# Kernel optimization log

Measured on AMD Instinct MI355X. Metric: run time of the kernel, lower is better.

Reference implementation:

```python
import jax, jax.numpy as jnp
import numpy as np
import math

MAX_P = 150
D_MODEL = 128
N_HEADS = 4
D_HEAD = D_MODEL // N_HEADS
D_MLP = 512
D_MEM = 64
VOCAB = MAX_P + 2  # 152
EQ_TOKEN = MAX_P + 1  # 151
B = 65536


def setup_inputs() -> dict:
    key = jax.random.key(0)
    ks = jax.random.split(key, 20)
    s = 1.0 / math.sqrt(D_MODEL)
    inp = {
        "p_val": jax.random.randint(ks[0], (B,), 0, MAX_P),
        "a": jax.random.randint(ks[1], (B,), 0, MAX_P),
        "b": jax.random.randint(ks[2], (B,), 0, MAX_P),
        # embeddings
        "token_embed": jax.random.normal(ks[3], (VOCAB, D_MODEL), jnp.float32),
        "pos_embed": jax.random.normal(ks[4], (5, D_MODEL), jnp.float32),
        # TitansMemory
        "W_mem": jax.random.normal(ks[5], (D_MODEL, D_MEM), jnp.float32) * s,
        "b_mem": jnp.zeros((D_MEM,), jnp.float32),
        "W_sur": jax.random.normal(ks[6], (D_MEM, D_MODEL), jnp.float32) * (1.0 / math.sqrt(D_MEM)),
        "b_sur": jnp.zeros((D_MODEL,), jnp.float32),
        "W_m2r": jax.random.normal(ks[7], (D_MEM, D_MODEL), jnp.float32) * (1.0 / math.sqrt(D_MEM)),
        "b_m2r": jnp.zeros((D_MODEL,), jnp.float32),
        # attention
        "W_Q": jax.random.normal(ks[8], (N_HEADS, D_MODEL, D_HEAD), jnp.float32) * s,
        "W_K": jax.random.normal(ks[9], (N_HEADS, D_MODEL, D_HEAD), jnp.float32) * s,
        "W_V": jax.random.normal(ks[10], (N_HEADS, D_MODEL, D_HEAD), jnp.float32) * s,
        "W_O": jax.random.normal(ks[11], (N_HEADS, D_HEAD, D_MODEL), jnp.float32) * s,
        # MLP
        "W_mlp1": jax.random.normal(ks[12], (D_MODEL, D_MLP), jnp.float32) * s,
        "b_mlp1": jnp.zeros((D_MLP,), jnp.float32),
        "W_mlp2": jax.random.normal(ks[13], (D_MLP, D_MODEL), jnp.float32) * (1.0 / math.sqrt(D_MLP)),
        "b_mlp2": jnp.zeros((D_MODEL,), jnp.float32),
        # unembed
        "W_un": jax.random.normal(ks[14], (D_MODEL, MAX_P), jnp.float32) * s,
        "b_un": jnp.zeros((MAX_P,), jnp.float32),
    }
    return inp


def reference(p_val, a, b, token_embed, pos_embed, W_mem, b_mem, W_sur, b_sur,
              W_m2r, b_m2r, W_Q, W_K, W_V, W_O, W_mlp1, b_mlp1, W_mlp2, b_mlp2,
              W_un, b_un):
    eq = jnp.full_like(a, EQ_TOKEN)
    tokens = jnp.stack([p_val, a, b, eq], axis=1)            # [B, 4]
    x = token_embed[tokens] + pos_embed[:4][None, :, :]       # [B, 4, D]

    # Titans memory (test-time update) on the modulus token embedding
    x0 = x[:, 0, :]                                           # [B, D]
    z = jax.nn.silu(x0 @ W_mem + b_mem)                       # [B, d_mem]
    pred_x = z @ W_sur + b_sur                                # [B, D]
    update = jax.nn.silu((x0 - pred_x) @ W_mem)               # [B, d_mem]
    mem = (z + update) @ W_m2r + b_m2r                        # [B, D]
    x = x + mem[:, None, :]

    # attention
    q = jnp.einsum('bsd,hdk->bhsk', x, W_Q)
    k = jnp.einsum('bsd,hdk->bhsk', x, W_K)
    v = jnp.einsum('bsd,hdk->bhsk', x, W_V)
    scores = jnp.einsum('bhsk,bhtk->bhst', q, k) / math.sqrt(D_HEAD)
    pattern = jax.nn.softmax(scores, axis=-1)                 # [B, H, 4, 4]
    attn = jnp.einsum('bhst,bhtk->bhsk', pattern, v)
    attn = jnp.einsum('bhsk,hkm->bsm', attn, W_O)             # [B, 4, D]
    x = x + attn

    # MLP
    x = x + jax.nn.relu(x @ W_mlp1 + b_mlp1) @ W_mlp2 + b_mlp2

    # unembed the '=' position
    logits = x[:, 3, :] @ W_un + b_un                         # [B, max_p]
    return logits
```

## Files before the change

kernel.cpp:

```cpp
#include <hip/hip_runtime.h>

#define D      128
#define DM     64
#define DMLP   512
#define PMAX   150
#define VOC    152
#define EQT    151
#define NBATCH 65536

typedef __attribute__((ext_vector_type(8))) __bf16 bf16x8;
typedef __attribute__((ext_vector_type(4))) float  f32x4;

__device__ __forceinline__ float silu_f(float x){ return x / (1.0f + expf(-x)); }

#define OFF_MEMVEC 0
#define OFF_X3BASE 19200
#define OFF_KE     19328
#define OFF_KP     38784
#define OFF_SC     39296
#define OFF_O0     132896
#define OFF_O1     171296
#define OFF_O2     209696
#define OFF_O3     248096
#define OFF_M3B    248352
#define OFF_W1F    257952
#define OFF_W2F    290720
#define OFF_WUF    323488

__global__ void k_P1a(const float* __restrict__ tok, const float* __restrict__ pos,
                      const float* __restrict__ W_mem, const float* __restrict__ b_mem,
                      const float* __restrict__ W_sur, const float* __restrict__ b_sur,
                      const float* __restrict__ W_m2r, const float* __restrict__ b_m2r,
                      const float* __restrict__ W_K,
                      float* __restrict__ memvec, float* __restrict__ x3base,
                      float* __restrict__ KE, float* __restrict__ KP)
{
    int r = blockIdx.x, t = threadIdx.x;
    if (r < 150) {
        int p = r;
        __shared__ float sx0[D], sz[DM], sdiff[D], szu[DM];
        if (t < D) sx0[t] = tok[p*D + t] + pos[t];
        __syncthreads();
        if (t < DM) {
            float acc = b_mem[t];
            for (int d = 0; d < D; d++) acc += sx0[d] * W_mem[d*DM + t];
            sz[t] = silu_f(acc);
        }
        __syncthreads();
        if (t < D) {
            float acc = b_sur[t];
            for (int j = 0; j < DM; j++) acc += sz[j] * W_sur[j*D + t];
            sdiff[t] = sx0[t] - acc;
        }
        __syncthreads();
        if (t < DM) {
            float acc = 0.f;
            for (int d = 0; d < D; d++) acc += sdiff[d] * W_mem[d*DM + t];
            szu[t] = sz[t] + silu_f(acc);
        }
        __syncthreads();
        if (t < D) {
            float acc = b_m2r[t];
            for (int j = 0; j < DM; j++) acc += szu[j] * W_m2r[j*D + t];
            memvec[p*D + t] = acc;
        }
    } else if (r == 150) {
        if (t < D) x3base[t] = tok[EQT*D + t] + pos[3*D + t];
    } else {
        int idx = r - 151;
        const float* src = (idx < 152) ? (tok + idx*D) : (pos + (idx-152)*D);
        float*       dst = (idx < 152) ? (KE + idx*D)  : (KP + (idx-152)*D);
        __shared__ float s[D];
        if (t < D) s[t] = src[t];
        __syncthreads();
        if (t < D) {
            int h = t >> 5, k = t & 31;
            float acc = 0.f;
            for (int d = 0; d < D; d++) acc += s[d] * W_K[h*4096 + d*32 + k];
            dst[t] = acc;
        }
    }
}

__global__ void k_P2x(const float* __restrict__ memvec, const float* __restrict__ x3base,
                      const float* __restrict__ W_Q, const float* __restrict__ W_V,
                      const float* __restrict__ W_O,
                      const float* __restrict__ KE, const float* __restrict__ KP,
                      const float* __restrict__ tok, const float* __restrict__ pos,
                      const float* __restrict__ W1, const float* __restrict__ W2,
                      const float* __restrict__ WU,
                      float* __restrict__ SC, __bf16* __restrict__ M3B,
                      __bf16* __restrict__ O0, __bf16* __restrict__ O1,
                      __bf16* __restrict__ O2, __bf16* __restrict__ O3,
                      __bf16* __restrict__ W1f, __bf16* __restrict__ W2f, __bf16* __restrict__ WUf)
{
    int r = blockIdx.x, t = threadIdx.x;
    if (r < 300) {
        int p = r >> 1, half = r & 1;
        __shared__ float sMem[D], sIn[D], sQ3[D], sMV[D];
        if (t < D) { float m = memvec[p*D + t]; sMem[t] = m; sIn[t] = m + x3base[t]; }
        __syncthreads();
        if (t < D) {
            int h = t >> 5, k = t & 31;
            float acc = 0.f;
            for (int d = 0; d < D; d++) acc += sIn[d] * W_Q[h*4096 + d*32 + k];
            sQ3[t] = acc;
        } else {
            int c = t - D; int h = c >> 5, k = c & 31;
            float acc = 0.f;
            for (int d = 0; d < D; d++) acc += sMem[d] * W_V[h*4096 + d*32 + k];
            sMV[c] = acc;
        }
        __syncthreads();
        const float scale = 0.17677669529663687f;
        for (int ii = t; ii < 312; ii += 256) {
            int i = half*312 + ii;
            int v = i >> 2, h = i & 3;
            const float4* qh = (const float4*)(sQ3 + h*32);
            float4 s4 = {0.f, 0.f, 0.f, 0.f};
            if (v < 152) {
                const float4* ke = (const float4*)(KE + v*D + h*32);
                #pragma unroll
                for (int k = 0; k < 8; k++) {
                    float4 q = qh[k], e = ke[k];
                    s4.x += q.x*e.x; s4.y += q.y*e.y; s4.z += q.z*e.z; s4.w += q.w*e.w;
                }
            } else if (v == 152 || v == 153) {
                const float4* ke = (const float4*)(KE + ((v==152)? p : EQT)*D + h*32);
                const float4* kp = (const float4*)(KP + ((v==152)? 0 : 3)*D + h*32);
                #pragma unroll
                for (int k = 0; k < 8; k++) {
                    float4 q = qh[k], e = ke[k], pp = kp[k];
                    s4.x += q.x*(e.x+pp.x); s4.y += q.y*(e.y+pp.y);
                    s4.z += q.z*(e.z+pp.z); s4.w += q.w*(e.w+pp.w);
                }
            } else {
                const float4* kp = (const float4*)(KP + ((v==154)?1:2)*D + h*32);
                #pragma unroll
                for (int k = 0; k < 8; k++) {
                    float4 q = qh[k], pp = kp[k];
                    s4.x += q.x*pp.x; s4.y += q.y*pp.y; s4.z += q.z*pp.z; s4.w += q.w*pp.w;
                }
            }
            SC[p*624 + i] = (s4.x + s4.y + s4.z + s4.w) * scale;
        }
        if (half == 0 && t < D) {
            float acc = sIn[t];
            for (int c = 0; c < D; c++) acc += sMV[c] * W_O[c*D + t];
            M3B[p*D + t] = (__bf16)acc;
        }
        return;
    }
    int rr = r - 300;
    if (rr < 451) {
        int idx = rr;
        int tt, v; __bf16* outp;
        if (idx < 150)      { tt = 0; v = idx;       outp = O0 + v*512; }
        else if (idx < 300) { tt = 1; v = idx - 150; outp = O1 + (idx-150)*512; }
        else if (idx < 450) { tt = 2; v = idx - 300; outp = O2 + (idx-300)*512; }
        else                { tt = 3; v = EQT;       outp = O3; }
        __shared__ float sTP[D], sv[D];
        if (t < D) sTP[t] = tok[v*D + t] + pos[tt*D + t];
        __syncthreads();
        if (t < D) {
            int h = t >> 5, k = t & 31;
            float acc = 0.f;
            for (int d = 0; d < D; d++) acc += sTP[d] * W_V[h*4096 + d*32 + k];
            sv[t] = acc;
        }
        __syncthreads();
        #pragma unroll
        for (int i = 0; i < 2; i++) {
            int c = t + i*256;
            int h = c >> 7, m = c & 127;
            float acc = 0.f;
            for (int k = 0; k < 32; k++) acc += sv[h*32 + k] * W_O[h*4096 + k*128 + m];
            outp[c] = (__bf16)acc;
        }
    } else if (rr < 483) {
        int f = (rr-451)*256 + t;
        int l = f & 63, kb = (f>>6) & 3, nb = f >> 8;
        int k0 = kb*32 + (l>>4)*8, n = nb*16 + (l&15);
        #pragma unroll
        for (int j = 0; j < 8; j++) W1f[f*8 + j] = (__bf16)W1[(k0+j)*DMLP + n];
    } else if (rr < 515) {
        int f = (rr-483)*256 + t;
        int l = f & 63, g = f >> 6;
        int nb = g & 7, kb = g >> 3;
        int k0 = kb*32 + (l>>4)*8, n = nb*16 + (l&15);
        #pragma unroll
        for (int j = 0; j < 8; j++) W2f[f*8 + j] = (__bf16)W2[(k0+j)*D + n];
    } else {
        int f = (rr-515)*256 + t;
        int l = f & 63, kb = (f>>6) & 3, nb = f >> 8;
        int k0 = kb*32 + (l>>4)*8, n = nb*16 + (l&15);
        #pragma unroll
        for (int j = 0; j < 8; j++) WUf[f*8 + j] = (__bf16)((n < 150) ? WU[(k0+j)*150 + n] : 0.f);
    }
}

__global__ __launch_bounds__(256, 4) void k_fused(
    const int* __restrict__ p_val, const int* __restrict__ a_tok, const int* __restrict__ b_tok,
    const float* __restrict__ SC, const __bf16* __restrict__ O0, const __bf16* __restrict__ O1,
    const __bf16* __restrict__ O2, const __bf16* __restrict__ O3g, const __bf16* __restrict__ M3B,
    const __bf16* __restrict__ W1f, const __bf16* __restrict__ W2f, const __bf16* __restrict__ WUf,
    const float* __restrict__ b1, const float* __restrict__ b2, const float* __restrict__ bun,
    float* __restrict__ out)
{
    __shared__ __align__(16) char smem[36992];
    float* sB = (float*)(smem + 33792);
    char* sX3 = smem + 16384;

    int tid = threadIdx.x;
    int wv = tid >> 6, l = tid & 63, lr = l & 15, quad = l >> 4;
    int tbase = blockIdx.x * 64 + wv * 16;

    const char* gW1 = (const char*)W1f;
    const char* gW2 = (const char*)W2f;

    float4 v0, v1, v2, v3;
    {
        const float4* g1 = (const float4*)gW1;
        const float4* g2 = (const float4*)gW2;
        v0 = g1[tid]; v1 = g1[tid + 256]; v2 = g2[tid]; v3 = g2[tid + 256];
    }

    for (int i = tid; i < 512; i += 256) sB[i] = b1[i];
    if (tid < 128) sB[512 + tid] = b2[tid];
    if (tid < 160) sB[640 + tid] = bun[tid];

    {
        int s = tid >> 2, h = tid & 3;
        int gs = blockIdx.x * 64 + s;
        int p = p_val[gs], ta = a_tok[gs], tb = b_tok[gs];

        float wloc[4];
        {
            const float* SCp = SC + p*624;
            float sc0 = SCp[608 + h];
            float sc3 = SCp[612 + h];
            float sc1 = SCp[ta*4 + h] + SCp[616 + h];
            float sc2 = SCp[tb*4 + h] + SCp[620 + h];
            float mx = fmaxf(fmaxf(sc0, sc1), fmaxf(sc2, sc3));
            float e0 = expf(sc0-mx), e1 = expf(sc1-mx), e2 = expf(sc2-mx), e3 = expf(sc3-mx);
            float inv = 1.f / (e0 + e1 + e2 + e3);
            wloc[0] = e0*inv; wloc[1] = e1*inv; wloc[2] = e2*inv; wloc[3] = e3*inv;
        }
        float w[16];
        #pragma unroll
        for (int j = 0; j < 4; j++) w[h*4 + j] = wloc[j];
        #pragma unroll
        for (int m = 1; m < 4; m++) {
            int oh = h ^ m;
            #pragma unroll
            for (int j = 0; j < 4; j++) w[oh*4 + j] = __shfl_xor(wloc[j], m);
        }

        const bf16x8* m3v = (const bf16x8*)(M3B + p*128);
        const bf16x8* t0  = (const bf16x8*)(O0 + p*512);
        const bf16x8* t1  = (const bf16x8*)(O1 + ta*512);
        const bf16x8* t2  = (const bf16x8*)(O2 + tb*512);
        const bf16x8* t3  = (const bf16x8*)O3g;
        #pragma unroll
        for (int jj = 0; jj < 4; jj++) {
            int c8 = h*4 + jj;
            bf16x8 mv = m3v[c8];
            float v[8];
            #pragma unroll
            for (int e = 0; e < 8; e++) v[e] = (float)mv[e];
            #pragma unroll
            for (int hh = 0; hh < 4; hh++) {
                int o8 = hh*16 + c8;
                bf16x8 e0 = t0[o8], e1 = t1[o8], e2 = t2[o8], e3 = t3[o8];
                float w0 = w[hh*4+0], w1 = w[hh*4+1], w2 = w[hh*4+2], w3 = w[hh*4+3];
                #pragma unroll
                for (int e = 0; e < 8; e++)
                    v[e] += w0*(float)e0[e] + w1*(float)e1[e] + w2*(float)e2[e] + w3*(float)e3[e];
            }
            bf16x8 st;
            #pragma unroll
            for (int e = 0; e < 8; e++) st[e] = (__bf16)v[e];
            *(bf16x8*)(sX3 + s*256 + ((c8*16) ^ ((s&7)<<4))) = st;
        }
    }
    __syncthreads();

    bf16x8 a[4];
    {
        int arow = wv*16 + lr;
        #pragma unroll
        for (int kb = 0; kb < 4; kb++)
            a[kb] = *(const bf16x8*)(sX3 + arow*256 + ((kb*64 + quad*16) ^ ((lr&7)<<4)));
    }

    char* sPanC = smem + 16384 + wv*1280;

    f32x4 acc2[8];
    #pragma unroll
    for (int i = 0; i < 8; i++) acc2[i] = (f32x4){0.f, 0.f, 0.f, 0.f};

    for (int cc = 0; cc < 16; cc++) {
        {
            float4* d1 = (float4*)smem;
            float4* d2 = (float4*)(smem + 8192);
            d1[tid] = v0; d1[tid + 256] = v1; d2[tid] = v2; d2[tid + 256] = v3;
        }
        __syncthreads();
        if (cc < 15) {
            const float4* g1 = (const float4*)(gW1 + (cc+1)*8192);
            const float4* g2 = (const float4*)(gW2 + (cc+1)*8192);
            v0 = g1[tid]; v1 = g1[tid + 256]; v2 = g2[tid]; v3 = g2[tid + 256];
        }
        #pragma unroll
        for (int nbl = 0; nbl < 2; nbl++) {
            float bv = sB[cc*32 + nbl*16 + lr];
            f32x4 acc = (f32x4){bv, bv, bv, bv};
            #pragma unroll
            for (int kb = 0; kb < 4; kb++) {
                bf16x8 w1 = *(const bf16x8*)(smem + ((nbl*4 + kb)*64 + l)*16);
                acc = __builtin_amdgcn_mfma_f32_16x16x32_bf16(a[kb], w1, acc, 0, 0, 0);
            }
            #pragma unroll
            for (int r = 0; r < 4; r++)
                *(__bf16*)(sPanC + (((quad*4 + r)*40) + nbl*16 + lr)*2) = (__bf16)fmaxf(acc[r], 0.f);
        }
        {
            bf16x8 h = *(const bf16x8*)(sPanC + (lr*40 + quad*8)*2);
            #pragma unroll
            for (int nb2 = 0; nb2 < 8; nb2++) {
                bf16x8 w2 = *(const bf16x8*)(smem + 8192 + (nb2*64 + l)*16);
                acc2[nb2] = __builtin_amdgcn_mfma_f32_16x16x32_bf16(h, w2, acc2[nb2], 0, 0, 0);
            }
        }
        __syncthreads();
    }

    #pragma unroll
    for (int nb2 = 0; nb2 < 8; nb2++) {
        int kb = nb2 >> 1;
        bf16x8 bi;
        #pragma unroll
        for (int j = 0; j < 8; j++)
            bi[j] = (kb*32 + quad*8 + j == nb2*16 + lr) ? (__bf16)1.0f : (__bf16)0.0f;
        acc2[nb2] = __builtin_amdgcn_mfma_f32_16x16x32_bf16(a[kb], bi, acc2[nb2], 0, 0, 0);
    }

    char* sPanE = smem + 16384 + wv*4352;
    #pragma unroll
    for (int nb2 = 0; nb2 < 8; nb2++) {
        int n = nb2*16 + lr;
        float bv = sB[512 + n];
        #pragma unroll
        for (int r = 0; r < 4; r++) {
            float v = acc2[nb2][r] + bv;
            *(__bf16*)(sPanE + (((quad*4 + r)*136) + n)*2) = (__bf16)v;
        }
    }
    bf16x8 au[4];
    #pragma unroll
    for (int kb = 0; kb < 4; kb++)
        au[kb] = *(const bf16x8*)(sPanE + (lr*136 + kb*32 + quad*8)*2);

    const char* gWU = (const char*)WUf;
    #pragma unroll
    for (int q = 0; q < 3; q++) {
        if (q < 2) {
            const float4* g = (const float4*)(gWU + q*16384);
            float4 u0 = g[tid], u1 = g[tid+256], u2 = g[tid+512], u3 = g[tid+768];
            float4* dd = (float4*)smem;
            dd[tid] = u0; dd[tid+256] = u1; dd[tid+512] = u2; dd[tid+768] = u3;
        } else {
            const float4* g = (const float4*)(gWU + 32768);
            float4 u0 = g[tid], u1 = g[tid+256];
            float4* dd = (float4*)smem;
            dd[tid] = u0; dd[tid+256] = u1;
        }
        __syncthreads();
        int ntn = (q < 2) ? 4 : 2;
        for (int ntl = 0; ntl < ntn; ntl++) {
            int nt = q*4 + ntl;
            int n = nt*16 + lr;
            float bv = (n < 150) ? sB[640 + n] : 0.f;
            f32x4 acc = (f32x4){bv, bv, bv, bv};
            #pragma unroll
            for (int kb = 0; kb < 4; kb++) {
                bf16x8 wu = *(const bf16x8*)(smem + ((ntl*4 + kb)*64 + l)*16);
                acc = __builtin_amdgcn_mfma_f32_16x16x32_bf16(au[kb], wu, acc, 0, 0, 0);
            }
            if (n < 150) {
                #pragma unroll
                for (int r = 0; r < 4; r++) {
                    int rowg = tbase + quad*4 + r;
                    out[rowg*150 + n] = acc[r];
                }
            }
        }
        if (q < 2) __syncthreads();
    }
}

extern "C" void kernel_launch(void* const* d_in, const int* in_sizes, int n_in,
                              void* d_out, int out_size, void* d_ws, size_t ws_size,
                              hipStream_t stream) {
    const int*   p_val = (const int*)d_in[0];
    const int*   a_tok = (const int*)d_in[1];
    const int*   b_tok = (const int*)d_in[2];
    const float* tok   = (const float*)d_in[3];
    const float* pos   = (const float*)d_in[4];
    const float* W_mem = (const float*)d_in[5];
    const float* b_mem = (const float*)d_in[6];
    const float* W_sur = (const float*)d_in[7];
    const float* b_sur = (const float*)d_in[8];
    const float* W_m2r = (const float*)d_in[9];
    const float* b_m2r = (const float*)d_in[10];
    const float* W_Q   = (const float*)d_in[11];
    const float* W_K   = (const float*)d_in[12];
    const float* W_V   = (const float*)d_in[13];
    const float* W_O   = (const float*)d_in[14];
    const float* W1    = (const float*)d_in[15];
    const float* b1    = (const float*)d_in[16];
    const float* W2    = (const float*)d_in[17];
    const float* b2    = (const float*)d_in[18];
    const float* WU    = (const float*)d_in[19];
    const float* bun   = (const float*)d_in[20];
    float* out = (float*)d_out;

    float* ws = (float*)d_ws;
    float* memvec = ws + OFF_MEMVEC;
    float* x3base = ws + OFF_X3BASE;
    float* KE     = ws + OFF_KE;
    float* KP     = ws + OFF_KP;
    float* SC     = ws + OFF_SC;
    __bf16* O0    = (__bf16*)(ws + OFF_O0);
    __bf16* O1    = (__bf16*)(ws + OFF_O1);
    __bf16* O2    = (__bf16*)(ws + OFF_O2);
    __bf16* O3    = (__bf16*)(ws + OFF_O3);
    __bf16* M3B   = (__bf16*)(ws + OFF_M3B);
    __bf16* W1f   = (__bf16*)(ws + OFF_W1F);
    __bf16* W2f   = (__bf16*)(ws + OFF_W2F);
    __bf16* WUf   = (__bf16*)(ws + OFF_WUF);

    k_P1a<<<307, 256, 0, stream>>>(tok, pos, W_mem, b_mem, W_sur, b_sur, W_m2r, b_m2r,
                                   W_K, memvec, x3base, KE, KP);
    k_P2x<<<825, 256, 0, stream>>>(memvec, x3base, W_Q, W_V, W_O, KE, KP,
                                   tok, pos, W1, W2, WU,
                                   SC, M3B, O0, O1, O2, O3, W1f, W2f, WUf);
    k_fused<<<NBATCH/64, 256, 0, stream>>>(p_val, a_tok, b_tok, SC, O0, O1, O2, O3, M3B,
                                           W1f, W2f, WUf, b1, b2, bun, out);
}
```

Measured before the change: 182.9 us.

## Make fused kernel wave-independent by reading weights directly from global memory

Removes block-wide shared-memory staging of the MLP and unembed weights and biases. Each wave now reads W1/W2/WU fragments and biases straight from global memory (expected to hit L1/L2) and uses a private 4 KB LDS slice for its activation panels, so all __syncthreads become per-wave waitcnt fences. This cuts LDS use from about 37 KB to 16 KB, which may raise occupancy and lets waves run without waiting on each other. In exchange, every wave issues its own global loads for the weight tiles, and nothing is prefetched, so MFMAs may stall on memory latency.

```diff
diff --git a/kernel.cpp b/kernel.cpp
--- a/kernel.cpp
+++ b/kernel.cpp
@@ -207,31 +207,16 @@
     const float* __restrict__ b1, const float* __restrict__ b2, const float* __restrict__ bun,
     float* __restrict__ out)
 {
-    __shared__ __align__(16) char smem[36992];
-    float* sB = (float*)(smem + 33792);
-    char* sX3 = smem + 16384;
+    __shared__ __align__(16) char smem[16384];
 
     int tid = threadIdx.x;
     int wv = tid >> 6, l = tid & 63, lr = l & 15, quad = l >> 4;
     int tbase = blockIdx.x * 64 + wv * 16;
-
-    const char* gW1 = (const char*)W1f;
-    const char* gW2 = (const char*)W2f;
-
-    float4 v0, v1, v2, v3;
+    char* sW = smem + wv*4096;
+
     {
-        const float4* g1 = (const float4*)gW1;
-        const float4* g2 = (const float4*)gW2;
-        v0 = g1[tid]; v1 = g1[tid + 256]; v2 = g2[tid]; v3 = g2[tid + 256];
-    }
-
-    for (int i = tid; i < 512; i += 256) sB[i] = b1[i];
-    if (tid < 128) sB[512 + tid] = b2[tid];
-    if (tid < 160) sB[640 + tid] = bun[tid];
-
-    {
-        int s = tid >> 2, h = tid & 3;
-        int gs = blockIdx.x * 64 + s;
+        int sl = l >> 2, h = l & 3;
+        int gs = tbase + sl;
         int p = p_val[gs], ta = a_tok[gs], tb = b_tok[gs];
 
         float wloc[4];
@@ -280,59 +265,47 @@
             bf16x8 st;
             #pragma unroll
             for (int e = 0; e < 8; e++) st[e] = (__bf16)v[e];
-            *(bf16x8*)(sX3 + s*256 + ((c8*16) ^ ((s&7)<<4))) = st;
-        }
-    }
-    __syncthreads();
+            *(bf16x8*)(sW + sl*256 + ((c8*16) ^ ((sl&7)<<4))) = st;
+        }
+    }
+    asm volatile("s_waitcnt lgkmcnt(0)" ::: "memory");
+    __builtin_amdgcn_sched_barrier(0);
 
     bf16x8 a[4];
-    {
-        int arow = wv*16 + lr;
-        #pragma unroll
-        for (int kb = 0; kb < 4; kb++)
-            a[kb] = *(const bf16x8*)(sX3 + arow*256 + ((kb*64 + quad*16) ^ ((lr&7)<<4)));
-    }
-
-    char* sPanC = smem + 16384 + wv*1280;
+    #pragma unroll
+    for (int kb = 0; kb < 4; kb++)
+        a[kb] = *(const bf16x8*)(sW + lr*256 + ((kb*64 + quad*16) ^ ((lr&7)<<4)));
+    asm volatile("s_waitcnt lgkmcnt(0)" ::: "memory");
+    __builtin_amdgcn_sched_barrier(0);
 
     f32x4 acc2[8];
     #pragma unroll
     for (int i = 0; i < 8; i++) acc2[i] = (f32x4){0.f, 0.f, 0.f, 0.f};
 
     for (int cc = 0; cc < 16; cc++) {
-        {
-            float4* d1 = (float4*)smem;
-            float4* d2 = (float4*)(smem + 8192);
-            d1[tid] = v0; d1[tid + 256] = v1; d2[tid] = v2; d2[tid + 256] = v3;
-        }
-        __syncthreads();
-        if (cc < 15) {
-            const float4* g1 = (const float4*)(gW1 + (cc+1)*8192);
-            const float4* g2 = (const float4*)(gW2 + (cc+1)*8192);
-            v0 = g1[tid]; v1 = g1[tid + 256]; v2 = g2[tid]; v3 = g2[tid + 256];
-        }
         #pragma unroll
         for (int nbl = 0; nbl < 2; nbl++) {
-            float bv = sB[cc*32 + nbl*16 + lr];
+            float bv = b1[cc*32 + nbl*16 + lr];
             f32x4 acc = (f32x4){bv, bv, bv, bv};
             #pragma unroll
             for (int kb = 0; kb < 4; kb++) {
-                bf16x8 w1 = *(const bf16x8*)(smem + ((nbl*4 + kb)*64 + l)*16);
+                bf16x8 w1 = *(const bf16x8*)(W1f + cc*4096 + ((nbl*4 + kb)*64 + l)*8);
                 acc = __builtin_amdgcn_mfma_f32_16x16x32_bf16(a[kb], w1, acc, 0, 0, 0);
             }
             #pragma unroll
             for (int r = 0; r < 4; r++)
-                *(__bf16*)(sPanC + (((quad*4 + r)*40) + nbl*16 + lr)*2) = (__bf16)fmaxf(acc[r], 0.f);
-        }
+                *(__bf16*)(sW + (((quad*4 + r)*40) + nbl*16 + lr)*2) = (__bf16)fmaxf(acc[r], 0.f);
+        }
+        asm volatile("s_waitcnt lgkmcnt(0)" ::: "memory");
+        __builtin_amdgcn_sched_barrier(0);
         {
-            bf16x8 h = *(const bf16x8*)(sPanC + (lr*40 + quad*8)*2);
+            bf16x8 h = *(const bf16x8*)(sW + (lr*40 + quad*8)*2);
             #pragma unroll
             for (int nb2 = 0; nb2 < 8; nb2++) {
-                bf16x8 w2 = *(const bf16x8*)(smem + 8192 + (nb2*64 + l)*16);
+                bf16x8 w2 = *(const bf16x8*)(W2f + cc*4096 + (nb2*64 + l)*8);
                 acc2[nb2] = __builtin_amdgcn_mfma_f32_16x16x32_bf16(h, w2, acc2[nb2], 0, 0, 0);
             }
         }
-        __syncthreads();
     }
 
     #pragma unroll
@@ -345,57 +318,40 @@
         acc2[nb2] = __builtin_amdgcn_mfma_f32_16x16x32_bf16(a[kb], bi, acc2[nb2], 0, 0, 0);
     }
 
-    char* sPanE = smem + 16384 + wv*4352;
     #pragma unroll
     for (int nb2 = 0; nb2 < 8; nb2++) {
         int n = nb2*16 + lr;
-        float bv = sB[512 + n];
+        float bv = b2[n];
         #pragma unroll
         for (int r = 0; r < 4; r++) {
             float v = acc2[nb2][r] + bv;
-            *(__bf16*)(sPanE + (((quad*4 + r)*136) + n)*2) = (__bf16)v;
-        }
-    }
+            int row = quad*4 + r;
+            *(__bf16*)(sW + row*256 + ((n*2) ^ ((row&7)<<4))) = (__bf16)v;
+        }
+    }
+    asm volatile("s_waitcnt lgkmcnt(0)" ::: "memory");
+    __builtin_amdgcn_sched_barrier(0);
     bf16x8 au[4];
     #pragma unroll
     for (int kb = 0; kb < 4; kb++)
-        au[kb] = *(const bf16x8*)(sPanE + (lr*136 + kb*32 + quad*8)*2);
-
-    const char* gWU = (const char*)WUf;
-    #pragma unroll
-    for (int q = 0; q < 3; q++) {
-        if (q < 2) {
-            const float4* g = (const float4*)(gWU + q*16384);
-            float4 u0 = g[tid], u1 = g[tid+256], u2 = g[tid+512], u3 = g[tid+768];
-            float4* dd = (float4*)smem;
-            dd[tid] = u0; dd[tid+256] = u1; dd[tid+512] = u2; dd[tid+768] = u3;
-        } else {
-            const float4* g = (const float4*)(gWU + 32768);
-            float4 u0 = g[tid], u1 = g[tid+256];
-            float4* dd = (float4*)smem;
-            dd[tid] = u0; dd[tid+256] = u1;
-        }
-        __syncthreads();
-        int ntn = (q < 2) ? 4 : 2;
-        for (int ntl = 0; ntl < ntn; ntl++) {
-            int nt = q*4 + ntl;
-            int n = nt*16 + lr;
-            float bv = (n < 150) ? sB[640 + n] : 0.f;
-            f32x4 acc = (f32x4){bv, bv, bv, bv};
-            #pragma unroll
-            for (int kb = 0; kb < 4; kb++) {
-                bf16x8 wu = *(const bf16x8*)(smem + ((ntl*4 + kb)*64 + l)*16);
-                acc = __builtin_amdgcn_mfma_f32_16x16x32_bf16(au[kb], wu, acc, 0, 0, 0);
+        au[kb] = *(const bf16x8*)(sW + lr*256 + ((kb*64 + quad*16) ^ ((lr&7)<<4)));
+
+    for (int nt = 0; nt < 10; nt++) {
+        int n = nt*16 + lr;
+        float bv = (n < 150) ? bun[n] : 0.f;
+        f32x4 acc = (f32x4){bv, bv, bv, bv};
+        #pragma unroll
+        for (int kb = 0; kb < 4; kb++) {
+            bf16x8 wu = *(const bf16x8*)(WUf + ((nt*4 + kb)*64 + l)*8);
+            acc = __builtin_amdgcn_mfma_f32_16x16x32_bf16(au[kb], wu, acc, 0, 0, 0);
+        }
+        if (n < 150) {
+            #pragma unroll
+            for (int r = 0; r < 4; r++) {
+                int rowg = tbase + quad*4 + r;
+                out[rowg*150 + n] = acc[r];
             }
-            if (n < 150) {
-                #pragma unroll
-                for (int r = 0; r < 4; r++) {
-                    int rowg = tbase + quad*4 + r;
-                    out[rowg*150 + n] = acc[r];
-                }
-            }
-        }
-        if (q < 2) __syncthreads();
+        }
     }
 }
 
```

Result: slower. 189.5 us (+3.6%).

## Double-buffer MLP weight chunks in LDS and drop shared bias staging

Applied to the files above, without the earlier changes.

Weight chunks for the MLP loop now go into two alternating LDS buffers. The next chunk is stored after the current chunk's MFMAs, so each iteration needs one barrier instead of two. Bias arrays are read straight from global memory instead of being staged in LDS. The post-MLP activation panel reuses the swizzled layout, and intra-wave LDS hazards are handled with waitcnt plus sched_barrier instead of block barriers. The trade-off is more LDS per block and global bias loads inside the inner loop.

```diff
diff --git a/kernel.cpp b/kernel.cpp
--- a/kernel.cpp
+++ b/kernel.cpp
@@ -207,8 +207,7 @@
     const float* __restrict__ b1, const float* __restrict__ b2, const float* __restrict__ bun,
     float* __restrict__ out)
 {
-    __shared__ __align__(16) char smem[36992];
-    float* sB = (float*)(smem + 33792);
+    __shared__ __align__(16) char smem[37888];
     char* sX3 = smem + 16384;
 
     int tid = threadIdx.x;
@@ -224,10 +223,6 @@
         const float4* g2 = (const float4*)gW2;
         v0 = g1[tid]; v1 = g1[tid + 256]; v2 = g2[tid]; v3 = g2[tid + 256];
     }
-
-    for (int i = tid; i < 512; i += 256) sB[i] = b1[i];
-    if (tid < 128) sB[512 + tid] = b2[tid];
-    if (tid < 160) sB[640 + tid] = bun[tid];
 
     {
         int s = tid >> 2, h = tid & 3;
@@ -283,7 +278,8 @@
             *(bf16x8*)(sX3 + s*256 + ((c8*16) ^ ((s&7)<<4))) = st;
         }
     }
-    __syncthreads();
+    asm volatile("s_waitcnt lgkmcnt(0)" ::: "memory");
+    __builtin_amdgcn_sched_barrier(0);
 
     bf16x8 a[4];
     {
@@ -292,20 +288,27 @@
         for (int kb = 0; kb < 4; kb++)
             a[kb] = *(const bf16x8*)(sX3 + arow*256 + ((kb*64 + quad*16) ^ ((lr&7)<<4)));
     }
-
-    char* sPanC = smem + 16384 + wv*1280;
+    {
+        float4* d1 = (float4*)smem;
+        d1[tid] = v0; d1[tid + 256] = v1;
+    }
+    __syncthreads();
+    {
+        float4* d2 = (float4*)(smem + 16384);
+        d2[tid] = v2; d2[tid + 256] = v3;
+    }
+    __syncthreads();
+
+    char* sPanH = smem + 32768 + wv*1280;
 
     f32x4 acc2[8];
     #pragma unroll
     for (int i = 0; i < 8; i++) acc2[i] = (f32x4){0.f, 0.f, 0.f, 0.f};
 
     for (int cc = 0; cc < 16; cc++) {
-        {
-            float4* d1 = (float4*)smem;
-            float4* d2 = (float4*)(smem + 8192);
-            d1[tid] = v0; d1[tid + 256] = v1; d2[tid] = v2; d2[tid + 256] = v3;
-        }
-        __syncthreads();
+        int p = cc & 1;
+        char* w1b = smem + p*8192;
+        char* w2b = smem + 16384 + p*8192;
         if (cc < 15) {
             const float4* g1 = (const float4*)(gW1 + (cc+1)*8192);
             const float4* g2 = (const float4*)(gW2 + (cc+1)*8192);
@@ -313,24 +316,31 @@
         }
         #pragma unroll
         for (int nbl = 0; nbl < 2; nbl++) {
-            float bv = sB[cc*32 + nbl*16 + lr];
+            float bv = b1[cc*32 + nbl*16 + lr];
             f32x4 acc = (f32x4){bv, bv, bv, bv};
             #pragma unroll
             for (int kb = 0; kb < 4; kb++) {
-                bf16x8 w1 = *(const bf16x8*)(smem + ((nbl*4 + kb)*64 + l)*16);
+                bf16x8 w1 = *(const bf16x8*)(w1b + ((nbl*4 + kb)*64 + l)*16);
                 acc = __builtin_amdgcn_mfma_f32_16x16x32_bf16(a[kb], w1, acc, 0, 0, 0);
             }
             #pragma unroll
             for (int r = 0; r < 4; r++)
-                *(__bf16*)(sPanC + (((quad*4 + r)*40) + nbl*16 + lr)*2) = (__bf16)fmaxf(acc[r], 0.f);
-        }
+                *(__bf16*)(sPanH + (((quad*4 + r)*40) + nbl*16 + lr)*2) = (__bf16)fmaxf(acc[r], 0.f);
+        }
+        asm volatile("s_waitcnt lgkmcnt(0)" ::: "memory");
+        __builtin_amdgcn_sched_barrier(0);
         {
-            bf16x8 h = *(const bf16x8*)(sPanC + (lr*40 + quad*8)*2);
+            bf16x8 h = *(const bf16x8*)(sPanH + (lr*40 + quad*8)*2);
             #pragma unroll
             for (int nb2 = 0; nb2 < 8; nb2++) {
-                bf16x8 w2 = *(const bf16x8*)(smem + 8192 + (nb2*64 + l)*16);
+                bf16x8 w2 = *(const bf16x8*)(w2b + (nb2*64 + l)*16);
                 acc2[nb2] = __builtin_amdgcn_mfma_f32_16x16x32_bf16(h, w2, acc2[nb2], 0, 0, 0);
             }
+        }
+        if (cc < 15) {
+            float4* d1 = (float4*)(smem + (p^1)*8192);
+            float4* d2 = (float4*)(smem + 16384 + (p^1)*8192);
+            d1[tid] = v0; d1[tid + 256] = v1; d2[tid] = v2; d2[tid + 256] = v3;
         }
         __syncthreads();
     }
@@ -345,34 +355,41 @@
         acc2[nb2] = __builtin_amdgcn_mfma_f32_16x16x32_bf16(a[kb], bi, acc2[nb2], 0, 0, 0);
     }
 
-    char* sPanE = smem + 16384 + wv*4352;
     #pragma unroll
     for (int nb2 = 0; nb2 < 8; nb2++) {
         int n = nb2*16 + lr;
-        float bv = sB[512 + n];
+        float bv = b2[n];
         #pragma unroll
         for (int r = 0; r < 4; r++) {
             float v = acc2[nb2][r] + bv;
-            *(__bf16*)(sPanE + (((quad*4 + r)*136) + n)*2) = (__bf16)v;
-        }
-    }
+            int row = wv*16 + quad*4 + r;
+            *(__bf16*)(smem + row*256 + ((n*2) ^ ((row&7)<<4))) = (__bf16)v;
+        }
+    }
+    asm volatile("s_waitcnt lgkmcnt(0)" ::: "memory");
+    __builtin_amdgcn_sched_barrier(0);
     bf16x8 au[4];
-    #pragma unroll
-    for (int kb = 0; kb < 4; kb++)
-        au[kb] = *(const bf16x8*)(sPanE + (lr*136 + kb*32 + quad*8)*2);
+    {
+        int arow = wv*16 + lr;
+        #pragma unroll
+        for (int kb = 0; kb < 4; kb++)
+            au[kb] = *(const bf16x8*)(smem + arow*256 + ((kb*64 + quad*16) ^ ((lr&7)<<4)));
+    }
 
     const char* gWU = (const char*)WUf;
+    char* sWU = smem + 16384;
     #pragma unroll
     for (int q = 0; q < 3; q++) {
+        __syncthreads();
         if (q < 2) {
             const float4* g = (const float4*)(gWU + q*16384);
             float4 u0 = g[tid], u1 = g[tid+256], u2 = g[tid+512], u3 = g[tid+768];
-            float4* dd = (float4*)smem;
+            float4* dd = (float4*)sWU;
             dd[tid] = u0; dd[tid+256] = u1; dd[tid+512] = u2; dd[tid+768] = u3;
         } else {
             const float4* g = (const float4*)(gWU + 32768);
             float4 u0 = g[tid], u1 = g[tid+256];
-            float4* dd = (float4*)smem;
+            float4* dd = (float4*)sWU;
             dd[tid] = u0; dd[tid+256] = u1;
         }
         __syncthreads();
@@ -380,11 +397,11 @@
         for (int ntl = 0; ntl < ntn; ntl++) {
             int nt = q*4 + ntl;
             int n = nt*16 + lr;
-            float bv = (n < 150) ? sB[640 + n] : 0.f;
+            float bv = (n < 150) ? bun[n] : 0.f;
             f32x4 acc = (f32x4){bv, bv, bv, bv};
             #pragma unroll
             for (int kb = 0; kb < 4; kb++) {
-                bf16x8 wu = *(const bf16x8*)(smem + ((ntl*4 + kb)*64 + l)*16);
+                bf16x8 wu = *(const bf16x8*)(sWU + ((ntl*4 + kb)*64 + l)*16);
                 acc = __builtin_amdgcn_mfma_f32_16x16x32_bf16(au[kb], wu, acc, 0, 0, 0);
             }
             if (n < 150) {
@@ -395,7 +412,6 @@
                 }
             }
         }
-        if (q < 2) __syncthreads();
     }
 }
 
```

Result: faster. 173.0 us (-5.4%).
